# Kernel tuning notes

Measured on AMD Instinct MI355X. Metric: run time of the kernel, lower is better.

## Reference

```python
import jax, jax.numpy as jnp
import numpy as np

B, N, M = 4, 8192, 8192


def setup_inputs() -> dict:
    key = jax.random.key(0)
    k1, k2, k3, k4 = jax.random.split(key, 4)
    xyz1 = jax.random.normal(k1, (B, N, 3), dtype=jnp.float32)
    xyz2 = jax.random.normal(k2, (B, M, 3), dtype=jnp.float32)
    weights1 = jax.random.uniform(k3, (B, N), dtype=jnp.float32)
    weights2 = jax.random.uniform(k4, (B, M), dtype=jnp.float32)
    return {"xyz1": xyz1, "xyz2": xyz2, "weights1": weights1, "weights2": weights2}


def _chamfer_dists(xyz1, xyz2):
    # Squared L2 pairwise distances via the ||a||^2 + ||b||^2 - 2 a.b identity
    # (avoids materializing a [B, N, M, 3] difference tensor).
    sq1 = jnp.sum(xyz1 * xyz1, axis=-1)            # [B, N]
    sq2 = jnp.sum(xyz2 * xyz2, axis=-1)            # [B, M]
    dots = jnp.einsum("bnc,bmc->bnm", xyz1, xyz2)  # [B, N, M]
    d = sq1[:, :, None] + sq2[:, None, :] - 2.0 * dots
    d = jnp.maximum(d, 0.0)
    dist1 = jnp.min(d, axis=2)  # [B, N] nearest in xyz2 for each point in xyz1
    dist2 = jnp.min(d, axis=1)  # [B, M] nearest in xyz1 for each point in xyz2
    return dist1, dist2


def reference(xyz1, xyz2, weights1, weights2):
    dist1, dist2 = _chamfer_dists(xyz1, xyz2)
    dist1 = dist1 * weights1
    dist2 = dist2 * weights2
    dist1_avg = jnp.sum(dist1) / jnp.sum(weights1)
    dist2_avg = jnp.sum(dist2) / jnp.sum(weights2)
    return (dist1_avg + dist2_avg) / 2.0
```

## Files before the change

kernel.cpp:

```cpp
#include <hip/hip_runtime.h>

#define TPBM 512
#define TPBR 1024
constexpr int Bsz  = 4;
constexpr int Npts = 8192;
constexpr int Mpts = 8192;
constexpr int PTS  = Bsz * Npts;
constexpr int QT_PER_B = Npts / 32;
constexpr int CT_PER_B = Mpts / 32;

typedef __attribute__((ext_vector_type(8)))  short short8;
typedef __attribute__((ext_vector_type(16))) float f32x16;

__device__ __forceinline__ float min3f(float a, float b, float c) {
    return fminf(fminf(a, b), c);
}

__device__ __forceinline__ f32x16 mfma_32x32(short8 a, short8 b) {
    f32x16 d;
    asm("v_mfma_f32_32x32x16_bf16 %0, %1, %2, 0\n\t"
        "s_nop 7\n\t"
        "s_nop 7\n\t"
        "s_nop 3"
        : "=&v"(d) : "v"(a), "v"(b));
    return d;
}

__device__ __forceinline__ unsigned short bfh(float v) {
    unsigned u = __float_as_uint(v);
    return (unsigned short)((u + 0x7fffu + ((u >> 16) & 1u)) >> 16);
}
__device__ __forceinline__ float b2f(unsigned short h) {
    return __uint_as_float(((unsigned)h) << 16);
}
__device__ __forceinline__ void split2(float v, unsigned short& h,
                                       unsigned short& m) {
    h = bfh(v); m = bfh(v - b2f(h));
}
__device__ __forceinline__ void split3(float v, unsigned short& h,
                                       unsigned short& m, unsigned short& l) {
    h = bfh(v); float fh = b2f(h);
    m = bfh(v - fh); float fm = b2f(m);
    l = bfh(v - fh - fm);
}

__device__ __forceinline__ short8 pack_frag(float x, float y, float z,
                                            int side, int g) {
    float n = fmaf(x, x, fmaf(y, y, z * z));
    float s = side ? 1.f : -2.f;
    unsigned short xh, xm, yh, ym, zh, zm, nh, nm, nl;
    split2(s * x, xh, xm);
    split2(s * y, yh, ym);
    split2(s * z, zh, zm);
    split3(n, nh, nm, nl);
    const unsigned short ONE = 0x3F80;
    short8 v;
#pragma unroll
    for (int j = 0; j < 8; ++j) {
        int k = g * 8 + j;
        unsigned short u = 0;
        if (k < 9) {
            int c = k / 3, o = k - 3 * c;
            unsigned short h = c == 0 ? xh : (c == 1 ? yh : zh);
            unsigned short m = c == 0 ? xm : (c == 1 ? ym : zm);
            u = side ? (o == 1 ? m : h)
                     : (o < 2 ? h : m);
        } else if (k < 12) {
            u = side ? ONE : (k == 9 ? nh : (k == 10 ? nm : nl));
        } else if (k < 15) {
            u = side ? (k == 12 ? nh : (k == 13 ? nm : nl)) : ONE;
        }
        v[j] = (short)u;
    }
    return v;
}

__global__ void __launch_bounds__(TPBM, 8) chamfer_fused_kernel(
    const float* __restrict__ xyz1, const float* __restrict__ xyz2,
    unsigned int* __restrict__ partials)
{
    int bid = blockIdx.x;
    int linear = (bid & 7) * 128 + (bid >> 3);
    int batch = linear >> 8;
    int rem = linear & 255;
    int qs = rem >> 3;
    int cs = rem & 7;
    int tid = threadIdx.x;
    int w = tid >> 6, lane = tid & 63;

    int qtile  = batch * QT_PER_B + qs * 8 + w;
    int ctile0 = batch * CT_PER_B + cs * 32;

    __shared__ short8 sc[2048];
    __shared__ unsigned int colb[1024];
    colb[tid]       = 0x7f7fffffu;
    colb[tid + 512] = 0x7f7fffffu;

#pragma unroll
    for (int i = 0; i < 4; ++i) {
        int e = tid + i * 512;
        int ct = e >> 6, ln = e & 63;
        int p = (ctile0 + ct) * 32 + (ln & 31);
        sc[e] = pack_frag(xyz2[p * 3 + 0], xyz2[p * 3 + 1], xyz2[p * 3 + 2],
                          1, ln >> 5);
    }

    short8 a;
    {
        int p = qtile * 32 + (lane & 31);
        a = pack_frag(xyz1[p * 3 + 0], xyz1[p * 3 + 1], xyz1[p * 3 + 2],
                      0, lane >> 5);
    }

    f32x16 rowp;
#pragma unroll
    for (int i = 0; i < 16; ++i) rowp[i] = 3.4e38f;
    __syncthreads();

    unsigned int* mycol = &colb[lane & 31];
    short8 b = sc[lane];

#pragma unroll 2
    for (int ct = 0; ct < 32; ++ct) {
        short8 bn = sc[((ct + 1) & 31) * 64 + lane];
        f32x16 d = mfma_32x32(a, b);
        rowp = __builtin_elementwise_min(rowp, d);
        float ca = min3f(d[0], d[1], d[2]);
        ca = min3f(ca, d[3], d[4]);
        ca = min3f(ca, d[5], d[6]);
        ca = fminf(ca, d[7]);
        float cb = min3f(d[8], d[9], d[10]);
        cb = min3f(cb, d[11], d[12]);
        cb = min3f(cb, d[13], d[14]);
        cb = fminf(cb, d[15]);
        atomicMin(mycol + ct * 32,
                  __float_as_uint(fmaxf(fminf(ca, cb), 0.f)));
        b = bn;
    }

#pragma unroll
    for (int i = 0; i < 16; ++i) {
        float v = rowp[i];
        v = fminf(v, __shfl_xor(v, 1));
        v = fminf(v, __shfl_xor(v, 2));
        v = fminf(v, __shfl_xor(v, 4));
        v = fminf(v, __shfl_xor(v, 8));
        v = fminf(v, __shfl_xor(v, 16));
        if ((lane & 31) == 0) {
            int row = (i & 3) + 4 * (lane >> 5) + 8 * (i >> 2);
            atomicMin(&partials[qtile * 32 + row],
                      __float_as_uint(fmaxf(v, 0.f)));
        }
    }

    __syncthreads();
    int cbase = PTS + ctile0 * 32;
    atomicMin(&partials[cbase + tid],       colb[tid]);
    atomicMin(&partials[cbase + tid + 512], colb[tid + 512]);
}

__global__ void __launch_bounds__(TPBR) reduce_final_kernel(
    const float* __restrict__ partials,
    const float* __restrict__ w1, const float* __restrict__ w2,
    float* __restrict__ out)
{
    int tid = threadIdx.x;
    const float4* d4 = (const float4*)partials;
    const float4* w14 = (const float4*)w1;
    const float4* w24 = (const float4*)w2;

    float c0 = 0.f, s0 = 0.f, c1 = 0.f, s1 = 0.f;
#pragma unroll
    for (int i = 0; i < 8; ++i) {
        int idx = tid + i * TPBR;
        float4 d = d4[idx], w = w14[idx];
        c0 += d.x * w.x + d.y * w.y + d.z * w.z + d.w * w.w;
        s0 += w.x + w.y + w.z + w.w;
    }
#pragma unroll
    for (int i = 0; i < 8; ++i) {
        int idx = tid + i * TPBR;
        float4 d = d4[8192 + idx], w = w24[idx];
        c1 += d.x * w.x + d.y * w.y + d.z * w.z + d.w * w.w;
        s1 += w.x + w.y + w.z + w.w;
    }

    for (int off = 32; off; off >>= 1) {
        c0 += __shfl_down(c0, off); s0 += __shfl_down(s0, off);
        c1 += __shfl_down(c1, off); s1 += __shfl_down(s1, off);
    }
    __shared__ float4 red[16];
    int lane = tid & 63, wid = tid >> 6;
    if (lane == 0) red[wid] = make_float4(c0, s0, c1, s1);
    __syncthreads();
    if (tid < 64) {
        float4 v = tid < 16 ? red[tid] : make_float4(0.f, 0.f, 0.f, 0.f);
        for (int off = 8; off; off >>= 1) {
            v.x += __shfl_down(v.x, off, 16);
            v.y += __shfl_down(v.y, off, 16);
            v.z += __shfl_down(v.z, off, 16);
            v.w += __shfl_down(v.w, off, 16);
        }
        if (tid == 0) out[0] = 0.5f * (v.x / v.y + v.z / v.w);
    }
}

extern "C" void kernel_launch(void* const* d_in, const int* in_sizes, int n_in,
                              void* d_out, int out_size, void* d_ws, size_t ws_size,
                              hipStream_t stream) {
    const float* xyz1 = (const float*)d_in[0];
    const float* xyz2 = (const float*)d_in[1];
    const float* w1   = (const float*)d_in[2];
    const float* w2   = (const float*)d_in[3];
    float* out = (float*)d_out;

    unsigned int* partials = (unsigned int*)d_ws;

    chamfer_fused_kernel<<<1024, TPBM, 0, stream>>>(xyz1, xyz2, partials);
    reduce_final_kernel<<<1, TPBR, 0, stream>>>((const float*)partials,
                                                w1, w2, out);
}
```

Before: 92.48 us.

## Split chamfer into two row-min passes instead of fused row/column mins

Replaces the single fused kernel, which computed row minima in registers and column minima through LDS atomics, with a doubled grid where each direction computes only row minima, swapping the roles of xyz1 and xyz2 for the second half. This removes the per-tile min-reduction tree and LDS atomicMin traffic from the inner loop, and each wave now starts at a staggered column tile. In exchange every distance MFMA runs twice, doubling tensor work and the packing of inputs. The change bets that the inner loop was limited by the column reduction and atomics rather than by MFMA throughput.

```diff
diff --git a/kernel.cpp b/kernel.cpp
--- a/kernel.cpp
+++ b/kernel.cpp
@@ -11,10 +11,6 @@
 
 typedef __attribute__((ext_vector_type(8)))  short short8;
 typedef __attribute__((ext_vector_type(16))) float f32x16;
-
-__device__ __forceinline__ float min3f(float a, float b, float c) {
-    return fminf(fminf(a, b), c);
-}
 
 __device__ __forceinline__ f32x16 mfma_32x32(short8 a, short8 b) {
     f32x16 d;
@@ -75,40 +71,42 @@
     return v;
 }
 
-__global__ void __launch_bounds__(TPBM, 8) chamfer_fused_kernel(
+__global__ void __launch_bounds__(TPBM, 8) chamfer_rows_kernel(
     const float* __restrict__ xyz1, const float* __restrict__ xyz2,
     unsigned int* __restrict__ partials)
 {
     int bid = blockIdx.x;
-    int linear = (bid & 7) * 128 + (bid >> 3);
-    int batch = linear >> 8;
-    int rem = linear & 255;
+    int linear = (bid & 7) * 256 + (bid >> 3);
+    int dir = linear >> 10;
+    int rem1024 = linear & 1023;
+    int batch = rem1024 >> 8;
+    int rem = rem1024 & 255;
     int qs = rem >> 3;
     int cs = rem & 7;
     int tid = threadIdx.x;
     int w = tid >> 6, lane = tid & 63;
 
+    const float* qsrc = dir ? xyz2 : xyz1;
+    const float* csrc = dir ? xyz1 : xyz2;
+
     int qtile  = batch * QT_PER_B + qs * 8 + w;
     int ctile0 = batch * CT_PER_B + cs * 32;
 
     __shared__ short8 sc[2048];
-    __shared__ unsigned int colb[1024];
-    colb[tid]       = 0x7f7fffffu;
-    colb[tid + 512] = 0x7f7fffffu;
 
 #pragma unroll
     for (int i = 0; i < 4; ++i) {
         int e = tid + i * 512;
         int ct = e >> 6, ln = e & 63;
         int p = (ctile0 + ct) * 32 + (ln & 31);
-        sc[e] = pack_frag(xyz2[p * 3 + 0], xyz2[p * 3 + 1], xyz2[p * 3 + 2],
+        sc[e] = pack_frag(csrc[p * 3 + 0], csrc[p * 3 + 1], csrc[p * 3 + 2],
                           1, ln >> 5);
     }
 
     short8 a;
     {
         int p = qtile * 32 + (lane & 31);
-        a = pack_frag(xyz1[p * 3 + 0], xyz1[p * 3 + 1], xyz1[p * 3 + 2],
+        a = pack_frag(qsrc[p * 3 + 0], qsrc[p * 3 + 1], qsrc[p * 3 + 2],
                       0, lane >> 5);
     }
 
@@ -117,25 +115,16 @@
     for (int i = 0; i < 16; ++i) rowp[i] = 3.4e38f;
     __syncthreads();
 
-    unsigned int* mycol = &colb[lane & 31];
-    short8 b = sc[lane];
+    int idx = (w * 4) & 31;
+    short8 b = sc[idx * 64 + lane];
 
 #pragma unroll 2
-    for (int ct = 0; ct < 32; ++ct) {
-        short8 bn = sc[((ct + 1) & 31) * 64 + lane];
+    for (int it = 0; it < 32; ++it) {
+        int nidx = (idx + 1) & 31;
+        short8 bn = sc[nidx * 64 + lane];
         f32x16 d = mfma_32x32(a, b);
         rowp = __builtin_elementwise_min(rowp, d);
-        float ca = min3f(d[0], d[1], d[2]);
-        ca = min3f(ca, d[3], d[4]);
-        ca = min3f(ca, d[5], d[6]);
-        ca = fminf(ca, d[7]);
-        float cb = min3f(d[8], d[9], d[10]);
-        cb = min3f(cb, d[11], d[12]);
-        cb = min3f(cb, d[13], d[14]);
-        cb = fminf(cb, d[15]);
-        atomicMin(mycol + ct * 32,
-                  __float_as_uint(fmaxf(fminf(ca, cb), 0.f)));
-        b = bn;
+        b = bn; idx = nidx;
     }
 
 #pragma unroll
@@ -148,15 +137,10 @@
         v = fminf(v, __shfl_xor(v, 16));
         if ((lane & 31) == 0) {
             int row = (i & 3) + 4 * (lane >> 5) + 8 * (i >> 2);
-            atomicMin(&partials[qtile * 32 + row],
+            atomicMin(&partials[dir * PTS + qtile * 32 + row],
                       __float_as_uint(fmaxf(v, 0.f)));
         }
     }
-
-    __syncthreads();
-    int cbase = PTS + ctile0 * 32;
-    atomicMin(&partials[cbase + tid],       colb[tid]);
-    atomicMin(&partials[cbase + tid + 512], colb[tid + 512]);
 }
 
 __global__ void __launch_bounds__(TPBR) reduce_final_kernel(
@@ -216,7 +200,7 @@
 
     unsigned int* partials = (unsigned int*)d_ws;
 
-    chamfer_fused_kernel<<<1024, TPBM, 0, stream>>>(xyz1, xyz2, partials);
+    chamfer_rows_kernel<<<2048, TPBM, 0, stream>>>(xyz1, xyz2, partials);
     reduce_final_kernel<<<1, TPBR, 0, stream>>>((const float*)partials,
                                                 w1, w2, out);
 }
```

Result: slower. 111.7 us (+20.8%).
